# Kernel tuning notes

Hardware: AMD Instinct MI355X
Metric: run time of the kernel (lower is better)

Reference implementation:

```python
import jax, jax.numpy as jnp
import numpy as np

TOP_K = 2

def setup_inputs() -> dict:
    key = jax.random.key(0)
    ks = jax.random.split(key, 6)
    B, S, D, H, E = 2, 1024, 512, 1024, 8
    x = jax.random.normal(ks[0], (B, S, D), dtype=jnp.float32)
    w_router = jax.random.normal(ks[1], (E, D), dtype=jnp.float32) / np.sqrt(D)
    b_router = jnp.zeros((E,), dtype=jnp.float32)
    w1 = jax.random.normal(ks[2], (E, H, D), dtype=jnp.float32) / np.sqrt(D)   # per-expert fc1 (hidden, in)
    w2 = jax.random.normal(ks[3], (E, D, H), dtype=jnp.float32) / np.sqrt(H)   # per-expert fc2 (out, hidden)
    return {"x": x, "w_router": w_router, "b_router": b_router, "w1": w1, "w2": w2}


def reference(x, w_router, b_router, w1, w2):
    B, S, D = x.shape
    E = w_router.shape[0]
    x_flat = x.reshape(-1, D)                                  # [T, D]
    # Router: logits -> softmax -> top-k -> renormalize -> dispatch weights
    router_logits = x_flat @ w_router.T + b_router             # [T, E]
    probs = jax.nn.softmax(router_logits, axis=-1)
    top_p, top_i = jax.lax.top_k(probs, TOP_K)                 # [T, K]
    top_p = top_p / jnp.sum(top_p, axis=-1, keepdims=True)
    # dispatch[t, e] = normalized prob if e in top-k of t else 0
    dispatch = jnp.sum(jax.nn.one_hot(top_i, E, dtype=x.dtype) * top_p[..., None], axis=1)  # [T, E]
    # Dense-masked expert MLP (mathematically identical to gather/GEMM/scatter):
    h = jax.nn.gelu(jnp.einsum('td,ehd->teh', x_flat, w1), approximate=False)  # [T, E, H]
    y = jnp.einsum('teh,edh->ted', h, w2)                      # [T, E, Dout]
    out = jnp.einsum('ted,te->td', y, dispatch)                # weighted combine
    out = out.reshape(B, S, -1)
    return out, router_logits
```

## Files before the change

kernel.cpp:

```cpp
#include <hip/hip_runtime.h>
#include <hip/hip_bf16.h>
#include <math.h>

#define T_TOK 2048
#define DIM 512
#define HID 1024
#define NE 8
#define CAP 1024

#define ROUT_BLKS 128
#define CAST_BLKS 2048

typedef __attribute__((ext_vector_type(8))) short short8;
typedef __attribute__((ext_vector_type(4))) float floatx4;

__device__ __forceinline__ unsigned short f2bf_bits(float f) {
    __hip_bfloat16 h = __float2bfloat16(f);
    return *reinterpret_cast<unsigned short*>(&h);
}

__device__ __forceinline__ float bf2f(unsigned short u) {
    unsigned int b = ((unsigned int)u) << 16;
    return *reinterpret_cast<float*>(&b);
}

__device__ __forceinline__ void gl2lds(const unsigned short* g, unsigned short* l) {
    __builtin_amdgcn_global_load_lds(
        (const __attribute__((address_space(1))) unsigned int*)g,
        (__attribute__((address_space(3))) unsigned int*)l, 16, 0, 0);
}

__device__ __forceinline__ short8 frag(const unsigned short* s, int row, int kg) {
    return *reinterpret_cast<const short8*>(s + row * 128 + (((kg) ^ (row & 7)) << 3));
}

template<int T>
__device__ __forceinline__ void stage_tile(const unsigned short* src, size_t RS,
                                           int k0, unsigned short* lds,
                                           int wave, int lane) {
    int ro = lane >> 4, gr = lane & 15;
#pragma unroll
    for (int i = wave; i < T / 4; i += 4) {
        int r = i * 4 + ro;
        gl2lds(src + (size_t)r * RS + k0 + (((gr ^ (r & 7)) << 3)),
               lds + i * 512);
    }
}

__global__ __launch_bounds__(256)
void prep(const float* __restrict__ x, const float* __restrict__ wr,
          const float* __restrict__ br,
          const float* __restrict__ w1, const float* __restrict__ w2,
          unsigned short* __restrict__ w1b, unsigned short* __restrict__ w2b,
          unsigned short* __restrict__ xg, int* __restrict__ counts,
          int2* __restrict__ pairSlot, float2* __restrict__ pw,
          float* __restrict__ logits_out) {
    int bx = blockIdx.x;
    int tid = threadIdx.x;
    if (bx >= ROUT_BLKS) {
        const int n1 = NE * HID * DIM / 4;
        int base = (bx - ROUT_BLKS) * 1024 + tid;
#pragma unroll
        for (int rep = 0; rep < 4; rep++) {
            int i = base + rep * 256;
            const float* s = (i < n1) ? w1 : w2;
            unsigned short* d = (i < n1) ? w1b : w2b;
            int j = (i < n1) ? i : i - n1;
            float4 v = reinterpret_cast<const float4*>(s)[j];
            ushort4 o;
            o.x = f2bf_bits(v.x); o.y = f2bf_bits(v.y);
            o.z = f2bf_bits(v.z); o.w = f2bf_bits(v.w);
            reinterpret_cast<ushort4*>(d)[j] = o;
        }
        return;
    }
    int wave = tid >> 6, lane = tid & 63;
    for (int it = 0; it < 4; it++) {
        int t = bx * 16 + it * 4 + wave;
        const float4* xr = reinterpret_cast<const float4*>(x + (size_t)t * DIM);
        float4 xa = xr[lane * 2], xc = xr[lane * 2 + 1];
        short8 o;
        o[0] = (short)f2bf_bits(xa.x); o[1] = (short)f2bf_bits(xa.y);
        o[2] = (short)f2bf_bits(xa.z); o[3] = (short)f2bf_bits(xa.w);
        o[4] = (short)f2bf_bits(xc.x); o[5] = (short)f2bf_bits(xc.y);
        o[6] = (short)f2bf_bits(xc.z); o[7] = (short)f2bf_bits(xc.w);
        float p[NE];
#pragma unroll
        for (int e = 0; e < NE; e++) {
            const float4* wre = reinterpret_cast<const float4*>(wr + e * DIM);
            float4 wa = wre[lane * 2], wc = wre[lane * 2 + 1];
            p[e] = xa.x * wa.x + xa.y * wa.y + xa.z * wa.z + xa.w * wa.w
                 + xc.x * wc.x + xc.y * wc.y + xc.z * wc.z + xc.w * wc.w;
        }
#pragma unroll
        for (int e = 0; e < NE; e++) {
#pragma unroll
            for (int off = 32; off >= 1; off >>= 1)
                p[e] += __shfl_xor(p[e], off, 64);
        }
        int slot1 = 0, slot2 = 0;
        if (lane == 0) {
            float l[NE];
#pragma unroll
            for (int e = 0; e < NE; e++) {
                l[e] = p[e] + br[e];
                logits_out[(size_t)t * NE + e] = l[e];
            }
            int e1 = 0;
#pragma unroll
            for (int e = 1; e < NE; e++) if (l[e] > l[e1]) e1 = e;
            int es = -1;
#pragma unroll
            for (int e = 0; e < NE; e++) {
                if (e == e1) continue;
                if (es < 0 || l[e] > l[es]) es = e;
            }
            float z = expf(l[es] - l[e1]);
            float inv = 1.f / (1.f + z);
            int pos1 = atomicAdd(&counts[e1 * 16], 1);
            if (pos1 > CAP - 1) pos1 = CAP - 1;
            int pos2 = atomicAdd(&counts[es * 16], 1);
            if (pos2 > CAP - 1) pos2 = CAP - 1;
            slot1 = e1 * CAP + pos1;
            slot2 = es * CAP + pos2;
            pairSlot[t] = make_int2(slot1, slot2);
            pw[t] = make_float2(inv, z * inv);
        }
        slot1 = __shfl(slot1, 0);
        slot2 = __shfl(slot2, 0);
        *reinterpret_cast<short8*>(xg + (size_t)slot1 * DIM + lane * 8) = o;
        *reinterpret_cast<short8*>(xg + (size_t)slot2 * DIM + lane * 8) = o;
    }
}

__global__ __launch_bounds__(256, 3)
void gemm1(const unsigned short* __restrict__ xg,
           const unsigned short* __restrict__ w1b,
           const int* __restrict__ counts,
           unsigned short* __restrict__ Hb) {
    int bx = blockIdx.x;
    int e = bx & 7;
    int rest = bx >> 3;
    int n0 = (rest & 7) * 128;
    int m0 = (rest >> 3) * 64;
    int cnt = counts[e * 16]; if (cnt > CAP) cnt = CAP;
    if (m0 >= cnt) return;

    __shared__ __align__(16) unsigned short s_a[64 * 128];
    __shared__ __align__(16) unsigned short s_b[128 * 128];

    int tid = threadIdx.x, wave = tid >> 6, lane = tid & 63;
    int g = lane >> 4, ln = lane & 15;
    int wm = wave & 1, wn = wave >> 1;

    const unsigned short* asrc = xg + (size_t)(e * CAP + m0) * DIM;
    const unsigned short* bsrc = w1b + (size_t)(e * HID + n0) * DIM;

    floatx4 acc[2][4];
#pragma unroll
    for (int mf = 0; mf < 2; mf++)
#pragma unroll
        for (int nf = 0; nf < 4; nf++) acc[mf][nf] = (floatx4){0.f, 0.f, 0.f, 0.f};

    for (int ph = 0; ph < 4; ph++) {
        int k0 = ph * 128;
        stage_tile<64>(asrc, DIM, k0, s_a, wave, lane);
        stage_tile<128>(bsrc, DIM, k0, s_b, wave, lane);
        __syncthreads();
#pragma unroll
        for (int ks = 0; ks < 4; ks++) {
            short8 a0 = frag(s_a, wm * 32 + ln, ks * 4 + g);
            short8 a1 = frag(s_a, wm * 32 + 16 + ln, ks * 4 + g);
#pragma unroll
            for (int nf = 0; nf < 4; nf++) {
                short8 b = frag(s_b, wn * 64 + nf * 16 + ln, ks * 4 + g);
                acc[0][nf] = __builtin_amdgcn_mfma_f32_16x16x32_bf16(a0, b, acc[0][nf], 0, 0, 0);
                acc[1][nf] = __builtin_amdgcn_mfma_f32_16x16x32_bf16(a1, b, acc[1][nf], 0, 0, 0);
            }
        }
        __syncthreads();
    }
#pragma unroll
    for (int mf = 0; mf < 2; mf++)
#pragma unroll
        for (int nf = 0; nf < 4; nf++)
#pragma unroll
            for (int r = 0; r < 4; r++) {
                int lr = wm * 32 + mf * 16 + g * 4 + r;
                int col = n0 + wn * 64 + nf * 16 + ln;
                float v = acc[mf][nf][r];
                float gv = 0.5f * v * (1.f + erff(v * 0.70710678118f));
                Hb[(size_t)(e * CAP + m0 + lr) * HID + col] = f2bf_bits(gv);
            }
}

__global__ __launch_bounds__(256, 3)
void gemm2(const unsigned short* __restrict__ Hb,
           const unsigned short* __restrict__ w2b,
           const int* __restrict__ counts,
           unsigned short* __restrict__ ybuf) {
    int bx = blockIdx.x;
    int e = bx & 7;
    int rest = bx >> 3;
    int n0 = (rest & 3) * 128;
    int kv = (rest >> 2) & 1;
    int m0 = (rest >> 3) * 64;
    int cnt = counts[e * 16]; if (cnt > CAP) cnt = CAP;
    if (m0 >= cnt) return;

    __shared__ __align__(16) unsigned short s_a[64 * 128];
    __shared__ __align__(16) unsigned short s_b[128 * 128];

    int tid = threadIdx.x, wave = tid >> 6, lane = tid & 63;
    int g = lane >> 4, ln = lane & 15;
    int wm = wave & 1, wn = wave >> 1;

    const unsigned short* asrc = Hb + (size_t)(e * CAP + m0) * HID;
    const unsigned short* bsrc = w2b + (size_t)(e * DIM + n0) * HID;

    floatx4 acc[2][4];
#pragma unroll
    for (int mf = 0; mf < 2; mf++)
#pragma unroll
        for (int nf = 0; nf < 4; nf++) acc[mf][nf] = (floatx4){0.f, 0.f, 0.f, 0.f};

    for (int ph = 0; ph < 4; ph++) {
        int k0 = kv * 512 + ph * 128;
        stage_tile<64>(asrc, HID, k0, s_a, wave, lane);
        stage_tile<128>(bsrc, HID, k0, s_b, wave, lane);
        __syncthreads();
#pragma unroll
        for (int ks = 0; ks < 4; ks++) {
            short8 a0 = frag(s_a, wm * 32 + ln, ks * 4 + g);
            short8 a1 = frag(s_a, wm * 32 + 16 + ln, ks * 4 + g);
#pragma unroll
            for (int nf = 0; nf < 4; nf++) {
                short8 b = frag(s_b, wn * 64 + nf * 16 + ln, ks * 4 + g);
                acc[0][nf] = __builtin_amdgcn_mfma_f32_16x16x32_bf16(a0, b, acc[0][nf], 0, 0, 0);
                acc[1][nf] = __builtin_amdgcn_mfma_f32_16x16x32_bf16(a1, b, acc[1][nf], 0, 0, 0);
            }
        }
        __syncthreads();
    }
    unsigned short* yb = ybuf + (size_t)kv * (NE * CAP * DIM);
#pragma unroll
    for (int mf = 0; mf < 2; mf++)
#pragma unroll
        for (int nf = 0; nf < 4; nf++)
#pragma unroll
            for (int r = 0; r < 4; r++) {
                int lr = wm * 32 + mf * 16 + g * 4 + r;
                int col = n0 + wn * 64 + nf * 16 + ln;
                yb[(size_t)(e * CAP + m0 + lr) * DIM + col] = f2bf_bits(acc[mf][nf][r]);
            }
}

__global__ __launch_bounds__(256)
void combine_kernel(const unsigned short* __restrict__ ybuf,
                    const int2* __restrict__ pairSlot,
                    const float2* __restrict__ pw, float* __restrict__ out) {
    int id = blockIdx.x * 256 + threadIdx.x;
    int t = id >> 6, d8 = (id & 63) * 8;
    int2 s = pairSlot[t];
    float2 w = pw[t];
    const size_t KV = (size_t)NE * CAP * DIM;
    short8 a = *reinterpret_cast<const short8*>(ybuf + (size_t)s.x * DIM + d8);
    short8 b = *reinterpret_cast<const short8*>(ybuf + KV + (size_t)s.x * DIM + d8);
    short8 c = *reinterpret_cast<const short8*>(ybuf + (size_t)s.y * DIM + d8);
    short8 d = *reinterpret_cast<const short8*>(ybuf + KV + (size_t)s.y * DIM + d8);
    float4 r0, r1;
    float* r = &r0.x;
#pragma unroll
    for (int j = 0; j < 8; j++) {
        float v = w.x * (bf2f((unsigned short)a[j]) + bf2f((unsigned short)b[j]))
                + w.y * (bf2f((unsigned short)c[j]) + bf2f((unsigned short)d[j]));
        if (j < 4) (&r0.x)[j] = v; else (&r1.x)[j - 4] = v;
    }
    (void)r;
    float4* dst = reinterpret_cast<float4*>(out + (size_t)t * DIM + d8);
    dst[0] = r0;
    dst[1] = r1;
}

extern "C" void kernel_launch(void* const* d_in, const int* in_sizes, int n_in,
                              void* d_out, int out_size, void* d_ws, size_t ws_size,
                              hipStream_t stream) {
    const float* x  = (const float*)d_in[0];
    const float* wr = (const float*)d_in[1];
    const float* br = (const float*)d_in[2];
    const float* w1 = (const float*)d_in[3];
    const float* w2 = (const float*)d_in[4];
    float* out = (float*)d_out;
    float* logits_out = out + (size_t)T_TOK * DIM;

    char* ws = (char*)d_ws;
    int*    counts   = (int*)ws;
    int2*   pairSlot = (int2*)(ws + 4096);
    float2* pw       = (float2*)(ws + 24576);
    unsigned short* xg  = (unsigned short*)(ws + 131072);
    unsigned short* w1b = (unsigned short*)(ws + 8519680);
    unsigned short* w2b = (unsigned short*)(ws + 16908288);
    unsigned short* Hb  = (unsigned short*)(ws + 25296896);
    unsigned short* ybuf = (unsigned short*)(ws + 42074112);

    hipMemsetAsync(counts, 0, 512, stream);

    prep<<<ROUT_BLKS + CAST_BLKS, 256, 0, stream>>>(
        x, wr, br, w1, w2, w1b, w2b, xg, counts, pairSlot, pw, logits_out);

    gemm1<<<NE * 16 * 8, 256, 0, stream>>>(xg, w1b, counts, Hb);

    gemm2<<<NE * 16 * 2 * 4, 256, 0, stream>>>(Hb, w2b, counts, ybuf);

    combine_kernel<<<512, 256, 0, stream>>>(ybuf, pairSlot, pw, out);
}
```

Baseline: 125.9 us.

## Fuse MoE pipeline into one persistent kernel with grid barriers and tile queues

Replaces the four separate launches (prep, gemm1, gemm2, combine) with a single persistent kernel of 512 blocks that uses atomic-counter grid barriers between phases. The GEMM phases pull tiles from atomic work queues, so blocks skip empty expert tiles and balance load dynamically. The goal is to remove launch gaps and tail idle time between kernels. The trade-off is spin-wait barrier overhead and a dependence on all 512 blocks being co-resident; at 3 blocks per CU, a device with enough CUs is needed or the barriers deadlock.

```diff
diff --git a/kernel.cpp b/kernel.cpp
--- a/kernel.cpp
+++ b/kernel.cpp
@@ -8,8 +8,11 @@
 #define NE 8
 #define CAP 1024
 
+#define GRID 512
 #define ROUT_BLKS 128
-#define CAST_BLKS 2048
+#define CAST_BLKS (GRID - ROUT_BLKS)
+#define G1_TILES (NE * 16 * 8)
+#define G2_TILES (NE * 16 * 2 * 4)
 
 typedef __attribute__((ext_vector_type(8))) short short8;
 typedef __attribute__((ext_vector_type(4))) float floatx4;
@@ -47,22 +50,103 @@
     }
 }
 
-__global__ __launch_bounds__(256)
-void prep(const float* __restrict__ x, const float* __restrict__ wr,
-          const float* __restrict__ br,
-          const float* __restrict__ w1, const float* __restrict__ w2,
-          unsigned short* __restrict__ w1b, unsigned short* __restrict__ w2b,
-          unsigned short* __restrict__ xg, int* __restrict__ counts,
-          int2* __restrict__ pairSlot, float2* __restrict__ pw,
-          float* __restrict__ logits_out) {
-    int bx = blockIdx.x;
-    int tid = threadIdx.x;
-    if (bx >= ROUT_BLKS) {
+__device__ __forceinline__ void gbar(int* ctr, int target) {
+    __syncthreads();
+    if (threadIdx.x == 0) {
+        __threadfence();
+        __hip_atomic_fetch_add(ctr, 1, __ATOMIC_RELEASE, __HIP_MEMORY_SCOPE_AGENT);
+        while (__hip_atomic_load(ctr, __ATOMIC_RELAXED, __HIP_MEMORY_SCOPE_AGENT) < target)
+            __builtin_amdgcn_s_sleep(2);
+    }
+    __syncthreads();
+    __threadfence();
+}
+
+__global__ __launch_bounds__(256, 3)
+void moe_mega(const float* __restrict__ x, const float* __restrict__ wr,
+              const float* __restrict__ br, const float* __restrict__ w1,
+              const float* __restrict__ w2,
+              unsigned short* __restrict__ w1b, unsigned short* __restrict__ w2b,
+              unsigned short* __restrict__ xg, int* __restrict__ fl,
+              int2* __restrict__ pairSlot, float2* __restrict__ pw,
+              unsigned short* __restrict__ Hb, unsigned short* __restrict__ ybuf,
+              float* __restrict__ out, float* __restrict__ logits_out) {
+    __shared__ __align__(16) unsigned short s_a[64 * 128];
+    __shared__ __align__(16) unsigned short s_b[128 * 128];
+    __shared__ int s_next;
+
+    const int bx = blockIdx.x, tid = threadIdx.x;
+    const int wave = tid >> 6, lane = tid & 63;
+    const int g = lane >> 4, ln = lane & 15;
+    const int wm = wave & 1, wn = wave >> 1;
+
+    int* counts = fl;
+    int* q1   = fl + 128;
+    int* q2   = fl + 129;
+    int* bar1 = fl + 160;
+    int* bar2 = fl + 192;
+    int* bar3 = fl + 224;
+
+    if (bx < ROUT_BLKS) {
+        for (int it = 0; it < 4; it++) {
+            int t = bx * 16 + it * 4 + wave;
+            const float4* xr = reinterpret_cast<const float4*>(x + (size_t)t * DIM);
+            float4 xa = xr[lane * 2], xc = xr[lane * 2 + 1];
+            short8 o;
+            o[0] = (short)f2bf_bits(xa.x); o[1] = (short)f2bf_bits(xa.y);
+            o[2] = (short)f2bf_bits(xa.z); o[3] = (short)f2bf_bits(xa.w);
+            o[4] = (short)f2bf_bits(xc.x); o[5] = (short)f2bf_bits(xc.y);
+            o[6] = (short)f2bf_bits(xc.z); o[7] = (short)f2bf_bits(xc.w);
+            float p[NE];
+#pragma unroll
+            for (int e = 0; e < NE; e++) {
+                const float4* wre = reinterpret_cast<const float4*>(wr + e * DIM);
+                float4 wa = wre[lane * 2], wc = wre[lane * 2 + 1];
+                p[e] = xa.x * wa.x + xa.y * wa.y + xa.z * wa.z + xa.w * wa.w
+                     + xc.x * wc.x + xc.y * wc.y + xc.z * wc.z + xc.w * wc.w;
+            }
+#pragma unroll
+            for (int e = 0; e < NE; e++) {
+#pragma unroll
+                for (int off = 32; off >= 1; off >>= 1)
+                    p[e] += __shfl_xor(p[e], off, 64);
+            }
+            int slot1 = 0, slot2 = 0;
+            if (lane == 0) {
+                float l[NE];
+#pragma unroll
+                for (int e = 0; e < NE; e++) {
+                    l[e] = p[e] + br[e];
+                    logits_out[(size_t)t * NE + e] = l[e];
+                }
+                int e1 = 0;
+#pragma unroll
+                for (int e = 1; e < NE; e++) if (l[e] > l[e1]) e1 = e;
+                int es = -1;
+#pragma unroll
+                for (int e = 0; e < NE; e++) {
+                    if (e == e1) continue;
+                    if (es < 0 || l[e] > l[es]) es = e;
+                }
+                float z = expf(l[es] - l[e1]);
+                float inv = 1.f / (1.f + z);
+                int pos1 = atomicAdd(&counts[e1 * 16], 1);
+                if (pos1 > CAP - 1) pos1 = CAP - 1;
+                int pos2 = atomicAdd(&counts[es * 16], 1);
+                if (pos2 > CAP - 1) pos2 = CAP - 1;
+                slot1 = e1 * CAP + pos1;
+                slot2 = es * CAP + pos2;
+                pairSlot[t] = make_int2(slot1, slot2);
+                pw[t] = make_float2(inv, z * inv);
+            }
+            slot1 = __shfl(slot1, 0);
+            slot2 = __shfl(slot2, 0);
+            *reinterpret_cast<short8*>(xg + (size_t)slot1 * DIM + lane * 8) = o;
+            *reinterpret_cast<short8*>(xg + (size_t)slot2 * DIM + lane * 8) = o;
+        }
+    } else {
         const int n1 = NE * HID * DIM / 4;
-        int base = (bx - ROUT_BLKS) * 1024 + tid;
-#pragma unroll
-        for (int rep = 0; rep < 4; rep++) {
-            int i = base + rep * 256;
+        for (int i = (bx - ROUT_BLKS) * 256 + tid; i < 2 * n1; i += CAST_BLKS * 256) {
             const float* s = (i < n1) ? w1 : w2;
             unsigned short* d = (i < n1) ? w1b : w2b;
             int j = (i < n1) ? i : i - n1;
@@ -72,214 +156,138 @@
             o.z = f2bf_bits(v.z); o.w = f2bf_bits(v.w);
             reinterpret_cast<ushort4*>(d)[j] = o;
         }
-        return;
-    }
-    int wave = tid >> 6, lane = tid & 63;
-    for (int it = 0; it < 4; it++) {
-        int t = bx * 16 + it * 4 + wave;
-        const float4* xr = reinterpret_cast<const float4*>(x + (size_t)t * DIM);
-        float4 xa = xr[lane * 2], xc = xr[lane * 2 + 1];
-        short8 o;
-        o[0] = (short)f2bf_bits(xa.x); o[1] = (short)f2bf_bits(xa.y);
-        o[2] = (short)f2bf_bits(xa.z); o[3] = (short)f2bf_bits(xa.w);
-        o[4] = (short)f2bf_bits(xc.x); o[5] = (short)f2bf_bits(xc.y);
-        o[6] = (short)f2bf_bits(xc.z); o[7] = (short)f2bf_bits(xc.w);
-        float p[NE];
-#pragma unroll
-        for (int e = 0; e < NE; e++) {
-            const float4* wre = reinterpret_cast<const float4*>(wr + e * DIM);
-            float4 wa = wre[lane * 2], wc = wre[lane * 2 + 1];
-            p[e] = xa.x * wa.x + xa.y * wa.y + xa.z * wa.z + xa.w * wa.w
-                 + xc.x * wc.x + xc.y * wc.y + xc.z * wc.z + xc.w * wc.w;
-        }
-#pragma unroll
-        for (int e = 0; e < NE; e++) {
-#pragma unroll
-            for (int off = 32; off >= 1; off >>= 1)
-                p[e] += __shfl_xor(p[e], off, 64);
-        }
-        int slot1 = 0, slot2 = 0;
-        if (lane == 0) {
-            float l[NE];
-#pragma unroll
-            for (int e = 0; e < NE; e++) {
-                l[e] = p[e] + br[e];
-                logits_out[(size_t)t * NE + e] = l[e];
-            }
-            int e1 = 0;
-#pragma unroll
-            for (int e = 1; e < NE; e++) if (l[e] > l[e1]) e1 = e;
-            int es = -1;
-#pragma unroll
-            for (int e = 0; e < NE; e++) {
-                if (e == e1) continue;
-                if (es < 0 || l[e] > l[es]) es = e;
-            }
-            float z = expf(l[es] - l[e1]);
-            float inv = 1.f / (1.f + z);
-            int pos1 = atomicAdd(&counts[e1 * 16], 1);
-            if (pos1 > CAP - 1) pos1 = CAP - 1;
-            int pos2 = atomicAdd(&counts[es * 16], 1);
-            if (pos2 > CAP - 1) pos2 = CAP - 1;
-            slot1 = e1 * CAP + pos1;
-            slot2 = es * CAP + pos2;
-            pairSlot[t] = make_int2(slot1, slot2);
-            pw[t] = make_float2(inv, z * inv);
-        }
-        slot1 = __shfl(slot1, 0);
-        slot2 = __shfl(slot2, 0);
-        *reinterpret_cast<short8*>(xg + (size_t)slot1 * DIM + lane * 8) = o;
-        *reinterpret_cast<short8*>(xg + (size_t)slot2 * DIM + lane * 8) = o;
-    }
-}
-
-__global__ __launch_bounds__(256, 3)
-void gemm1(const unsigned short* __restrict__ xg,
-           const unsigned short* __restrict__ w1b,
-           const int* __restrict__ counts,
-           unsigned short* __restrict__ Hb) {
-    int bx = blockIdx.x;
-    int e = bx & 7;
-    int rest = bx >> 3;
-    int n0 = (rest & 7) * 128;
-    int m0 = (rest >> 3) * 64;
-    int cnt = counts[e * 16]; if (cnt > CAP) cnt = CAP;
-    if (m0 >= cnt) return;
-
-    __shared__ __align__(16) unsigned short s_a[64 * 128];
-    __shared__ __align__(16) unsigned short s_b[128 * 128];
-
-    int tid = threadIdx.x, wave = tid >> 6, lane = tid & 63;
-    int g = lane >> 4, ln = lane & 15;
-    int wm = wave & 1, wn = wave >> 1;
-
-    const unsigned short* asrc = xg + (size_t)(e * CAP + m0) * DIM;
-    const unsigned short* bsrc = w1b + (size_t)(e * HID + n0) * DIM;
-
-    floatx4 acc[2][4];
-#pragma unroll
-    for (int mf = 0; mf < 2; mf++)
-#pragma unroll
-        for (int nf = 0; nf < 4; nf++) acc[mf][nf] = (floatx4){0.f, 0.f, 0.f, 0.f};
-
-    for (int ph = 0; ph < 4; ph++) {
-        int k0 = ph * 128;
-        stage_tile<64>(asrc, DIM, k0, s_a, wave, lane);
-        stage_tile<128>(bsrc, DIM, k0, s_b, wave, lane);
+    }
+    gbar(bar1, GRID);
+
+    while (true) {
+        if (tid == 0)
+            s_next = __hip_atomic_fetch_add(q1, 1, __ATOMIC_RELAXED, __HIP_MEMORY_SCOPE_AGENT);
         __syncthreads();
-#pragma unroll
-        for (int ks = 0; ks < 4; ks++) {
-            short8 a0 = frag(s_a, wm * 32 + ln, ks * 4 + g);
-            short8 a1 = frag(s_a, wm * 32 + 16 + ln, ks * 4 + g);
-#pragma unroll
-            for (int nf = 0; nf < 4; nf++) {
-                short8 b = frag(s_b, wn * 64 + nf * 16 + ln, ks * 4 + g);
-                acc[0][nf] = __builtin_amdgcn_mfma_f32_16x16x32_bf16(a0, b, acc[0][nf], 0, 0, 0);
-                acc[1][nf] = __builtin_amdgcn_mfma_f32_16x16x32_bf16(a1, b, acc[1][nf], 0, 0, 0);
-            }
+        int t5 = s_next;
+        if (t5 >= G1_TILES) break;
+        int e = t5 & 7;
+        int rest = t5 >> 3;
+        int n0 = (rest & 7) * 128;
+        int m0 = (rest >> 3) * 64;
+        int cnt = counts[e * 16]; if (cnt > CAP) cnt = CAP;
+        if (m0 < cnt) {
+            const unsigned short* asrc = xg + (size_t)(e * CAP + m0) * DIM;
+            const unsigned short* bsrc = w1b + (size_t)(e * HID + n0) * DIM;
+            floatx4 acc[2][4];
+#pragma unroll
+            for (int mf = 0; mf < 2; mf++)
+#pragma unroll
+                for (int nf = 0; nf < 4; nf++) acc[mf][nf] = (floatx4){0.f, 0.f, 0.f, 0.f};
+            for (int ph = 0; ph < 4; ph++) {
+                int k0 = ph * 128;
+                stage_tile<64>(asrc, DIM, k0, s_a, wave, lane);
+                stage_tile<128>(bsrc, DIM, k0, s_b, wave, lane);
+                __syncthreads();
+#pragma unroll
+                for (int ks = 0; ks < 4; ks++) {
+                    short8 a0 = frag(s_a, wm * 32 + ln, ks * 4 + g);
+                    short8 a1 = frag(s_a, wm * 32 + 16 + ln, ks * 4 + g);
+#pragma unroll
+                    for (int nf = 0; nf < 4; nf++) {
+                        short8 b = frag(s_b, wn * 64 + nf * 16 + ln, ks * 4 + g);
+                        acc[0][nf] = __builtin_amdgcn_mfma_f32_16x16x32_bf16(a0, b, acc[0][nf], 0, 0, 0);
+                        acc[1][nf] = __builtin_amdgcn_mfma_f32_16x16x32_bf16(a1, b, acc[1][nf], 0, 0, 0);
+                    }
+                }
+                __syncthreads();
+            }
+#pragma unroll
+            for (int mf = 0; mf < 2; mf++)
+#pragma unroll
+                for (int nf = 0; nf < 4; nf++)
+#pragma unroll
+                    for (int r = 0; r < 4; r++) {
+                        int lr = wm * 32 + mf * 16 + g * 4 + r;
+                        int col = n0 + wn * 64 + nf * 16 + ln;
+                        float v = acc[mf][nf][r];
+                        float gv = 0.5f * v * (1.f + erff(v * 0.70710678118f));
+                        Hb[(size_t)(e * CAP + m0 + lr) * HID + col] = f2bf_bits(gv);
+                    }
         }
         __syncthreads();
     }
-#pragma unroll
-    for (int mf = 0; mf < 2; mf++)
-#pragma unroll
-        for (int nf = 0; nf < 4; nf++)
-#pragma unroll
-            for (int r = 0; r < 4; r++) {
-                int lr = wm * 32 + mf * 16 + g * 4 + r;
-                int col = n0 + wn * 64 + nf * 16 + ln;
-                float v = acc[mf][nf][r];
-                float gv = 0.5f * v * (1.f + erff(v * 0.70710678118f));
-                Hb[(size_t)(e * CAP + m0 + lr) * HID + col] = f2bf_bits(gv);
-            }
-}
-
-__global__ __launch_bounds__(256, 3)
-void gemm2(const unsigned short* __restrict__ Hb,
-           const unsigned short* __restrict__ w2b,
-           const int* __restrict__ counts,
-           unsigned short* __restrict__ ybuf) {
-    int bx = blockIdx.x;
-    int e = bx & 7;
-    int rest = bx >> 3;
-    int n0 = (rest & 3) * 128;
-    int kv = (rest >> 2) & 1;
-    int m0 = (rest >> 3) * 64;
-    int cnt = counts[e * 16]; if (cnt > CAP) cnt = CAP;
-    if (m0 >= cnt) return;
-
-    __shared__ __align__(16) unsigned short s_a[64 * 128];
-    __shared__ __align__(16) unsigned short s_b[128 * 128];
-
-    int tid = threadIdx.x, wave = tid >> 6, lane = tid & 63;
-    int g = lane >> 4, ln = lane & 15;
-    int wm = wave & 1, wn = wave >> 1;
-
-    const unsigned short* asrc = Hb + (size_t)(e * CAP + m0) * HID;
-    const unsigned short* bsrc = w2b + (size_t)(e * DIM + n0) * HID;
-
-    floatx4 acc[2][4];
-#pragma unroll
-    for (int mf = 0; mf < 2; mf++)
-#pragma unroll
-        for (int nf = 0; nf < 4; nf++) acc[mf][nf] = (floatx4){0.f, 0.f, 0.f, 0.f};
-
-    for (int ph = 0; ph < 4; ph++) {
-        int k0 = kv * 512 + ph * 128;
-        stage_tile<64>(asrc, HID, k0, s_a, wave, lane);
-        stage_tile<128>(bsrc, HID, k0, s_b, wave, lane);
+    gbar(bar2, GRID);
+
+    while (true) {
+        if (tid == 0)
+            s_next = __hip_atomic_fetch_add(q2, 1, __ATOMIC_RELAXED, __HIP_MEMORY_SCOPE_AGENT);
         __syncthreads();
-#pragma unroll
-        for (int ks = 0; ks < 4; ks++) {
-            short8 a0 = frag(s_a, wm * 32 + ln, ks * 4 + g);
-            short8 a1 = frag(s_a, wm * 32 + 16 + ln, ks * 4 + g);
-#pragma unroll
-            for (int nf = 0; nf < 4; nf++) {
-                short8 b = frag(s_b, wn * 64 + nf * 16 + ln, ks * 4 + g);
-                acc[0][nf] = __builtin_amdgcn_mfma_f32_16x16x32_bf16(a0, b, acc[0][nf], 0, 0, 0);
-                acc[1][nf] = __builtin_amdgcn_mfma_f32_16x16x32_bf16(a1, b, acc[1][nf], 0, 0, 0);
-            }
+        int t6 = s_next;
+        if (t6 >= G2_TILES) break;
+        int e = t6 & 7;
+        int rest = t6 >> 3;
+        int n0 = (rest & 3) * 128;
+        int kv = (rest >> 2) & 1;
+        int m0 = (rest >> 3) * 64;
+        int cnt = counts[e * 16]; if (cnt > CAP) cnt = CAP;
+        if (m0 < cnt) {
+            const unsigned short* asrc = Hb + (size_t)(e * CAP + m0) * HID;
+            const unsigned short* bsrc = w2b + (size_t)(e * DIM + n0) * HID;
+            floatx4 acc[2][4];
+#pragma unroll
+            for (int mf = 0; mf < 2; mf++)
+#pragma unroll
+                for (int nf = 0; nf < 4; nf++) acc[mf][nf] = (floatx4){0.f, 0.f, 0.f, 0.f};
+            for (int ph = 0; ph < 4; ph++) {
+                int k0 = kv * 512 + ph * 128;
+                stage_tile<64>(asrc, HID, k0, s_a, wave, lane);
+                stage_tile<128>(bsrc, HID, k0, s_b, wave, lane);
+                __syncthreads();
+#pragma unroll
+                for (int ks = 0; ks < 4; ks++) {
+                    short8 a0 = frag(s_a, wm * 32 + ln, ks * 4 + g);
+                    short8 a1 = frag(s_a, wm * 32 + 16 + ln, ks * 4 + g);
+#pragma unroll
+                    for (int nf = 0; nf < 4; nf++) {
+                        short8 b = frag(s_b, wn * 64 + nf * 16 + ln, ks * 4 + g);
+                        acc[0][nf] = __builtin_amdgcn_mfma_f32_16x16x32_bf16(a0, b, acc[0][nf], 0, 0, 0);
+                        acc[1][nf] = __builtin_amdgcn_mfma_f32_16x16x32_bf16(a1, b, acc[1][nf], 0, 0, 0);
+                    }
+                }
+                __syncthreads();
+            }
+            unsigned short* yb = ybuf + (size_t)kv * (NE * CAP * DIM);
+#pragma unroll
+            for (int mf = 0; mf < 2; mf++)
+#pragma unroll
+                for (int nf = 0; nf < 4; nf++)
+#pragma unroll
+                    for (int r = 0; r < 4; r++) {
+                        int lr = wm * 32 + mf * 16 + g * 4 + r;
+                        int col = n0 + wn * 64 + nf * 16 + ln;
+                        yb[(size_t)(e * CAP + m0 + lr) * DIM + col] = f2bf_bits(acc[mf][nf][r]);
+                    }
         }
         __syncthreads();
     }
-    unsigned short* yb = ybuf + (size_t)kv * (NE * CAP * DIM);
-#pragma unroll
-    for (int mf = 0; mf < 2; mf++)
-#pragma unroll
-        for (int nf = 0; nf < 4; nf++)
-#pragma unroll
-            for (int r = 0; r < 4; r++) {
-                int lr = wm * 32 + mf * 16 + g * 4 + r;
-                int col = n0 + wn * 64 + nf * 16 + ln;
-                yb[(size_t)(e * CAP + m0 + lr) * DIM + col] = f2bf_bits(acc[mf][nf][r]);
-            }
-}
-
-__global__ __launch_bounds__(256)
-void combine_kernel(const unsigned short* __restrict__ ybuf,
-                    const int2* __restrict__ pairSlot,
-                    const float2* __restrict__ pw, float* __restrict__ out) {
-    int id = blockIdx.x * 256 + threadIdx.x;
-    int t = id >> 6, d8 = (id & 63) * 8;
-    int2 s = pairSlot[t];
-    float2 w = pw[t];
-    const size_t KV = (size_t)NE * CAP * DIM;
-    short8 a = *reinterpret_cast<const short8*>(ybuf + (size_t)s.x * DIM + d8);
-    short8 b = *reinterpret_cast<const short8*>(ybuf + KV + (size_t)s.x * DIM + d8);
-    short8 c = *reinterpret_cast<const short8*>(ybuf + (size_t)s.y * DIM + d8);
-    short8 d = *reinterpret_cast<const short8*>(ybuf + KV + (size_t)s.y * DIM + d8);
-    float4 r0, r1;
-    float* r = &r0.x;
-#pragma unroll
-    for (int j = 0; j < 8; j++) {
-        float v = w.x * (bf2f((unsigned short)a[j]) + bf2f((unsigned short)b[j]))
-                + w.y * (bf2f((unsigned short)c[j]) + bf2f((unsigned short)d[j]));
-        if (j < 4) (&r0.x)[j] = v; else (&r1.x)[j - 4] = v;
-    }
-    (void)r;
-    float4* dst = reinterpret_cast<float4*>(out + (size_t)t * DIM + d8);
-    dst[0] = r0;
-    dst[1] = r1;
+    gbar(bar3, GRID);
+
+    {
+        int id = bx * 256 + tid;
+        int t = id >> 6, d8 = (id & 63) * 8;
+        int2 s = pairSlot[t];
+        float2 w = pw[t];
+        const size_t KV = (size_t)NE * CAP * DIM;
+        short8 a = *reinterpret_cast<const short8*>(ybuf + (size_t)s.x * DIM + d8);
+        short8 b = *reinterpret_cast<const short8*>(ybuf + KV + (size_t)s.x * DIM + d8);
+        short8 c = *reinterpret_cast<const short8*>(ybuf + (size_t)s.y * DIM + d8);
+        short8 d = *reinterpret_cast<const short8*>(ybuf + KV + (size_t)s.y * DIM + d8);
+        float4 r0, r1;
+#pragma unroll
+        for (int j = 0; j < 8; j++) {
+            float v = w.x * (bf2f((unsigned short)a[j]) + bf2f((unsigned short)b[j]))
+                    + w.y * (bf2f((unsigned short)c[j]) + bf2f((unsigned short)d[j]));
+            if (j < 4) (&r0.x)[j] = v; else (&r1.x)[j - 4] = v;
+        }
+        float4* dst = reinterpret_cast<float4*>(out + (size_t)t * DIM + d8);
+        dst[0] = r0;
+        dst[1] = r1;
+    }
 }
 
 extern "C" void kernel_launch(void* const* d_in, const int* in_sizes, int n_in,
@@ -294,7 +302,7 @@
     float* logits_out = out + (size_t)T_TOK * DIM;
 
     char* ws = (char*)d_ws;
-    int*    counts   = (int*)ws;
+    int*    fl       = (int*)ws;
     int2*   pairSlot = (int2*)(ws + 4096);
     float2* pw       = (float2*)(ws + 24576);
     unsigned short* xg  = (unsigned short*)(ws + 131072);
@@ -303,14 +311,9 @@
     unsigned short* Hb  = (unsigned short*)(ws + 25296896);
     unsigned short* ybuf = (unsigned short*)(ws + 42074112);
 
-    hipMemsetAsync(counts, 0, 512, stream);
-
-    prep<<<ROUT_BLKS + CAST_BLKS, 256, 0, stream>>>(
-        x, wr, br, w1, w2, w1b, w2b, xg, counts, pairSlot, pw, logits_out);
-
-    gemm1<<<NE * 16 * 8, 256, 0, stream>>>(xg, w1b, counts, Hb);
-
-    gemm2<<<NE * 16 * 2 * 4, 256, 0, stream>>>(Hb, w2b, counts, ybuf);
-
-    combine_kernel<<<512, 256, 0, stream>>>(ybuf, pairSlot, pw, out);
-}
+    hipMemsetAsync(fl, 0, 4096, stream);
+
+    moe_mega<<<GRID, 256, 0, stream>>>(
+        x, wr, br, w1, w2, w1b, w2b, xg, fl, pairSlot, pw, Hb, ybuf,
+        out, logits_out);
+}
```

Result: slower. 363.3 us (+188.6%).
